# Optimization experiments

Hardware: AMD Instinct MI355X
Metric: run time of the kernel (lower is better)

Reference implementation:

```python
import jax, jax.numpy as jnp
from jax import lax
import numpy as np

B, T, C = 32, 1024, 512
K = 3
MAX_DUR = 4            # durations drawn from [0,5) -> max value 4
L_MAX = T * MAX_DUR    # static padded mel length (torch pads to batch max; we pad to static max)
EPS = 1e-5


def conv_ln_block(x, w, b, g, beta):
    # x: [B,T,C]; torch ConvLNBlock: permute -> Conv1d(SAME) -> relu -> permute -> LayerNorm -> dropout(eval=id)
    y = lax.conv_general_dilated(x.transpose(0, 2, 1), w, (1,), 'SAME',
                                 dimension_numbers=('NCH', 'OIH', 'NCH')) + b[None, :, None]
    y = jax.nn.relu(y).transpose(0, 2, 1)  # [B,T,Cout]
    mu = y.mean(-1, keepdims=True)
    var = y.var(-1, keepdims=True)
    return (y - mu) * lax.rsqrt(var + EPS) * g + beta


def regulate(batch, durations, token_lengths):
    # Vectorized equivalent of DurationRegulator.inflate: repeat token t durations[b,t] times,
    # concatenate, pad. Implemented as cumsum + searchsorted gather (single pass, no ragged loops).
    pos = jnp.arange(T)
    valid = pos[None, :] < token_lengths[:, None]          # [B,T]
    d = jnp.where(valid, durations, 0)
    total = d.sum(axis=1)
    # torch: if durs.sum()==0 -> fill with 1
    d = jnp.where((total == 0)[:, None], valid.astype(d.dtype), d)
    total = d.sum(axis=1)                                   # [B]
    cum = jnp.cumsum(d, axis=1)                             # inclusive cumsum [B,T]
    frames = jnp.arange(L_MAX)
    idx = jax.vmap(lambda c: jnp.searchsorted(c, frames, side='right'))(cum)  # [B,L_MAX]
    idx = jnp.clip(idx, 0, T - 1)
    out = jnp.take_along_axis(batch, idx[:, :, None], axis=1)                 # [B,L_MAX,C]
    frame_mask = frames[None, :] < total[:, None]
    out = out * frame_mask[:, :, None].astype(batch.dtype)
    return out, total.astype(jnp.float32)


def setup_inputs() -> dict:
    key = jax.random.key(0)
    ks = jax.random.split(key, 8)
    batch = jax.random.normal(ks[0], (B, T, C), dtype=jnp.float32)
    token_lengths = jax.random.randint(ks[1], (B,), T // 2, T + 1).astype(jnp.int32)
    mask = jnp.arange(T)[None, :] < token_lengths[:, None]
    label_durations = jax.random.randint(ks[2], (B, T), 0, MAX_DUR + 1).astype(jnp.int32)
    s1 = 1.0 / np.sqrt(C * K)
    s2 = 1.0 / np.sqrt(C * K)
    params = {
        'conv1_w': jax.random.uniform(ks[3], (C, C, K), minval=-s1, maxval=s1, dtype=jnp.float32),
        'conv1_b': jnp.zeros((C,), jnp.float32),
        'ln1_g': jnp.ones((C,), jnp.float32), 'ln1_b': jnp.zeros((C,), jnp.float32),
        'conv2_w': jax.random.uniform(ks[4], (C, C, K), minval=-s2, maxval=s2, dtype=jnp.float32),
        'conv2_b': jnp.zeros((C,), jnp.float32),
        'ln2_g': jnp.ones((C,), jnp.float32), 'ln2_b': jnp.zeros((C,), jnp.float32),
        'lin_w': jax.random.uniform(ks[5], (C, 1), minval=-1/np.sqrt(C), maxval=1/np.sqrt(C), dtype=jnp.float32),
        'lin_b': jnp.zeros((1,), jnp.float32),
    }
    return dict(batch=batch, token_lengths=token_lengths, mask=mask,
                label_durations=label_durations, **params)


def reference(batch, token_lengths, mask, label_durations,
              conv1_w, conv1_b, ln1_g, ln1_b,
              conv2_w, conv2_b, ln2_g, ln2_b,
              lin_w, lin_b):
    # VariancePredictor: two ConvLN blocks + Linear(out_channels, 1), masked fill 0
    h = conv_ln_block(batch, conv1_w, conv1_b, ln1_g, ln1_b)
    h = conv_ln_block(h, conv2_w, conv2_b, ln2_g, ln2_b)
    predicted_durations = h @ lin_w + lin_b                      # [B,T,1]
    predicted_durations = jnp.where(mask[:, :, None], predicted_durations, 0.0)
    # label_durations provided -> regulator uses labels (training path), alpha=1
    padded_batch, mel_lengths = regulate(batch, label_durations, token_lengths)
    return padded_batch, mel_lengths, predicted_durations
```

## Files before the change

kernel.cpp:

```cpp
#include <hip/hip_runtime.h>
#include <hip/hip_bf16.h>
#include <stdint.h>


typedef _Float16 f16;
typedef _Float16 f16x8 __attribute__((ext_vector_type(8)));
typedef float f32x4 __attribute__((ext_vector_type(4)));

#define B_    32
#define T_    1024
#define TP_   1026
#define C_    512
#define LMAX_ 4096
#define KDIM  1536

#define XPAD_OFF   0u
#define H1PAD_OFF  33619968u
#define W1T_OFF    67239936u
#define W2T_OFF    68812800u
#define YWS_OFF    70385664u
#define TOT_OFF    137494528u
#define IDX_OFF    137495040u
#define GWL_OFF    138019328u
#define K12_OFF    138021376u
#define STAT2_OFF  138021888u

#define AS1C(p) ((const __attribute__((address_space(1))) void*)(p))
#define AS3(p)  ((__attribute__((address_space(3))) void*)(p))

__global__ __launch_bounds__(256) void prep_pad(const float* __restrict__ batch,
                                                f16* __restrict__ xpad,
                                                f16* __restrict__ h1pad) {
    int row = blockIdx.x * 4 + (threadIdx.x >> 6);
    int lane = threadIdx.x & 63;
    int b = row / TP_, tt = row % TP_;
    size_t dsto = (size_t)row * C_ + lane * 8;
    if (tt == 0 || tt == TP_ - 1) {
        f16x8 z = {};
        *(f16x8*)(xpad + dsto) = z;
        *(f16x8*)(h1pad + dsto) = z;
    } else {
        const float* src = batch + ((size_t)(b * T_ + tt - 1)) * C_ + lane * 8;
        float4 v0 = ((const float4*)src)[0];
        float4 v1 = ((const float4*)src)[1];
        f16x8 h;
        h[0] = (f16)v0.x; h[1] = (f16)v0.y; h[2] = (f16)v0.z; h[3] = (f16)v0.w;
        h[4] = (f16)v1.x; h[5] = (f16)v1.y; h[6] = (f16)v1.z; h[7] = (f16)v1.w;
        *(f16x8*)(xpad + dsto) = h;
    }
}

__global__ __launch_bounds__(256) void prep_w(const float* __restrict__ w1,
                                              const float* __restrict__ w2,
                                              f16* __restrict__ w1t,
                                              f16* __restrict__ w2t,
                                              const float* __restrict__ g2,
                                              const float* __restrict__ be2,
                                              const float* __restrict__ lw,
                                              float* __restrict__ gwl,
                                              float* __restrict__ k12) {
    int o = blockIdx.x;
    const float* w = blockIdx.y ? w2 : w1;
    f16* wt = blockIdx.y ? w2t : w1t;
    for (int j = threadIdx.x; j < KDIM; j += 256) {
        int tap = j >> 9, i = j & 511;
        wt[(size_t)o * KDIM + j] = (f16)w[(size_t)o * KDIM + i * 3 + tap];
    }
    if (blockIdx.x == 0 && blockIdx.y == 0) {
        __shared__ float rk[4][2];
        float k1 = 0.f, k2 = 0.f;
        for (int c = threadIdx.x; c < C_; c += 256) {
            float gw_ = g2[c] * lw[c];
            gwl[c] = gw_;
            k1 += gw_;
            k2 += be2[c] * lw[c];
        }
#pragma unroll
        for (int m = 32; m; m >>= 1) {
            k1 += __shfl_xor(k1, m, 64);
            k2 += __shfl_xor(k2, m, 64);
        }
        if ((threadIdx.x & 63) == 0) {
            rk[threadIdx.x >> 6][0] = k1;
            rk[threadIdx.x >> 6][1] = k2;
        }
        __syncthreads();
        if (threadIdx.x == 0) {
            k12[0] = rk[0][0] + rk[1][0] + rk[2][0] + rk[3][0];
            k12[1] = rk[0][1] + rk[1][1] + rk[2][1] + rk[3][1];
        }
    }
}

__global__ __launch_bounds__(1024) void scan_kernel(const int* __restrict__ dur,
                                                    const int* __restrict__ tlen,
                                                    int* __restrict__ idxarr,
                                                    int* __restrict__ total,
                                                    float* __restrict__ mel_out) {
    int b = blockIdx.x, t = threadIdx.x;
    __shared__ int sd[1024];
    __shared__ int sv[1024];
    int L = tlen[b];
    int valid = (t < L) ? 1 : 0;
    int d = valid ? dur[b * T_ + t] : 0;
    sd[t] = d; sv[t] = valid;
    __syncthreads();
    for (int off = 1; off < 1024; off <<= 1) {
        int x = 0, y = 0;
        if (t >= off) { x = sd[t - off]; y = sv[t - off]; }
        __syncthreads();
        sd[t] += x; sv[t] += y;
        __syncthreads();
    }
    int totd = sd[1023];
    int cur  = (totd == 0) ? sv[t] : sd[t];
    int prev = (t == 0) ? 0 : ((totd == 0) ? sv[t - 1] : sd[t - 1]);
    for (int f = prev; f < cur; f++) idxarr[b * LMAX_ + f] = t;
    if (t == 1023) {
        int tt = (totd == 0) ? sv[1023] : totd;
        total[b] = tt;
        mel_out[b] = (float)tt;
    }
}

template<int EPI>
__global__ __launch_bounds__(256, 2) void gemm_k(const f16* __restrict__ A,
                                                 const f16* __restrict__ Bw,
                                                 const float* __restrict__ bias,
                                                 f16* __restrict__ Y,
                                                 const float* __restrict__ gwl,
                                                 float4* __restrict__ stats) {
    __shared__ f16 As[128 * 64];
    __shared__ f16 Bs[256 * 64];
    const int tid = threadIdx.x;
    const int lane = tid & 63;
    const int w = tid >> 6;
    const int m0 = blockIdx.x * 128;
    const int n0 = blockIdx.y * 256;
    const int arow0 = (m0 >> 10) * TP_ + (m0 & 1023);
    const int wm = (w & 1) * 64;
    const int wn = (w >> 1) * 128;

    f32x4 acc[4][8];
#pragma unroll
    for (int i = 0; i < 4; i++)
#pragma unroll
        for (int j = 0; j < 8; j++) acc[i][j] = (f32x4){0.f, 0.f, 0.f, 0.f};

    const int lrow = lane >> 3;
    const int gran = (lane & 7) ^ lrow;
    const f16* aB = A + (size_t)(arow0 + lrow) * C_ + gran * 8;
    const f16* bB = Bw + (size_t)(n0 + lrow) * KDIM + gran * 8;

    for (int kk = 0; kk < KDIM; kk += 64) {
        __syncthreads();
#pragma unroll
        for (int i = 0; i < 4; i++) {
            const int rb = (w + i * 4) * 8;
            __builtin_amdgcn_global_load_lds(AS1C(aB + (size_t)rb * C_ + kk),
                                             AS3(&As[rb * 64]), 16, 0, 0);
        }
#pragma unroll
        for (int j = 0; j < 8; j++) {
            const int rb = (w + j * 4) * 8;
            __builtin_amdgcn_global_load_lds(AS1C(bB + (size_t)rb * KDIM + kk),
                                             AS3(&Bs[rb * 64]), 16, 0, 0);
        }
        __syncthreads();
#pragma unroll
        for (int ks = 0; ks < 2; ks++) {
            const int sl = ((ks << 2) + (lane >> 4)) ^ (lane & 7);
            f16x8 af[4], bf[8];
#pragma unroll
            for (int mi = 0; mi < 4; mi++)
                af[mi] = *(const f16x8*)&As[(wm + mi * 16 + (lane & 15)) * 64 + sl * 8];
#pragma unroll
            for (int ni = 0; ni < 8; ni++)
                bf[ni] = *(const f16x8*)&Bs[(wn + ni * 16 + (lane & 15)) * 64 + sl * 8];
#pragma unroll
            for (int mi = 0; mi < 4; mi++)
#pragma unroll
                for (int ni = 0; ni < 8; ni++)
                    acc[mi][ni] = __builtin_amdgcn_mfma_f32_16x16x32_f16(
                        af[mi], bf[ni], acc[mi][ni], 0, 0, 0);
        }
    }

    const int col = lane & 15;
    const int row4 = (lane >> 4) * 4;

    if (EPI == 0) {
#pragma unroll
        for (int ni = 0; ni < 8; ni++) {
            int n = n0 + wn + ni * 16 + col;
            float bn = bias[n];
#pragma unroll
            for (int mi = 0; mi < 4; mi++) {
#pragma unroll
                for (int r = 0; r < 4; r++) {
                    int m = m0 + wm + mi * 16 + row4 + r;
                    float v = acc[mi][ni][r] + bn;
                    Y[(size_t)m * C_ + n] = (f16)(v > 0.f ? v : 0.f);
                }
            }
        }
    } else {
        float bn[8], gw[8];
#pragma unroll
        for (int ni = 0; ni < 8; ni++) {
            int n = n0 + wn + ni * 16 + col;
            bn[ni] = bias[n];
            gw[ni] = gwl[n];
        }
        float s_[4][4], q_[4][4], u_[4][4];
#pragma unroll
        for (int mi = 0; mi < 4; mi++)
#pragma unroll
            for (int r = 0; r < 4; r++) { s_[mi][r] = 0.f; q_[mi][r] = 0.f; u_[mi][r] = 0.f; }
#pragma unroll
        for (int mi = 0; mi < 4; mi++)
#pragma unroll
            for (int ni = 0; ni < 8; ni++)
#pragma unroll
                for (int r = 0; r < 4; r++) {
                    float v = acc[mi][ni][r] + bn[ni];
                    v = v > 0.f ? v : 0.f;
                    s_[mi][r] += v;
                    q_[mi][r] += v * v;
                    u_[mi][r] += v * gw[ni];
                }
#pragma unroll
        for (int m = 8; m; m >>= 1)
#pragma unroll
            for (int mi = 0; mi < 4; mi++)
#pragma unroll
                for (int r = 0; r < 4; r++) {
                    s_[mi][r] += __shfl_xor(s_[mi][r], m, 64);
                    q_[mi][r] += __shfl_xor(q_[mi][r], m, 64);
                    u_[mi][r] += __shfl_xor(u_[mi][r], m, 64);
                }
        __syncthreads();
        float* red = (float*)As;
        if (col == 0) {
#pragma unroll
            for (int mi = 0; mi < 4; mi++)
#pragma unroll
                for (int r = 0; r < 4; r++) {
                    int row = wm + mi * 16 + row4 + r;
                    int idx = ((w >> 1) * 128 + row) * 3;
                    red[idx]     = s_[mi][r];
                    red[idx + 1] = q_[mi][r];
                    red[idx + 2] = u_[mi][r];
                }
        }
        __syncthreads();
        if (tid < 128) {
            float S = red[tid * 3]     + red[(128 + tid) * 3];
            float Q = red[tid * 3 + 1] + red[(128 + tid) * 3 + 1];
            float U = red[tid * 3 + 2] + red[(128 + tid) * 3 + 2];
            stats[(size_t)(m0 + tid) * 2 + blockIdx.y] = (float4){S, Q, U, 0.f};
        }
    }
}

__global__ __launch_bounds__(256) void ln_kernel(const f16* __restrict__ Y,
                                                 const float* __restrict__ g,
                                                 const float* __restrict__ be,
                                                 f16* __restrict__ hpad) {
    int row = blockIdx.x * 4 + (threadIdx.x >> 6);
    int lane = threadIdx.x & 63;
    f16x8 yv = *(const f16x8*)(Y + (size_t)row * C_ + lane * 8);
    float v[8];
#pragma unroll
    for (int i = 0; i < 8; i++) v[i] = (float)yv[i];
    float s = 0.f, q = 0.f;
#pragma unroll
    for (int i = 0; i < 8; i++) { s += v[i]; q += v[i] * v[i]; }
#pragma unroll
    for (int m = 32; m; m >>= 1) { s += __shfl_xor(s, m, 64); q += __shfl_xor(q, m, 64); }
    float mu = s * (1.f / 512.f);
    float x = q * (1.f / 512.f) - mu * mu + 1e-5f;
    float rs = rsqrtf(x);
    rs = rs * (1.5f - 0.5f * x * rs * rs);
    const float4 g0 = ((const float4*)g)[lane * 2], g1 = ((const float4*)g)[lane * 2 + 1];
    const float4 e0 = ((const float4*)be)[lane * 2], e1 = ((const float4*)be)[lane * 2 + 1];
    f16x8 h;
    h[0] = (f16)((v[0] - mu) * rs * g0.x + e0.x);
    h[1] = (f16)((v[1] - mu) * rs * g0.y + e0.y);
    h[2] = (f16)((v[2] - mu) * rs * g0.z + e0.z);
    h[3] = (f16)((v[3] - mu) * rs * g0.w + e0.w);
    h[4] = (f16)((v[4] - mu) * rs * g1.x + e1.x);
    h[5] = (f16)((v[5] - mu) * rs * g1.y + e1.y);
    h[6] = (f16)((v[6] - mu) * rs * g1.z + e1.z);
    h[7] = (f16)((v[7] - mu) * rs * g1.w + e1.w);
    int b = row >> 10, t = row & 1023;
    *(f16x8*)(hpad + ((size_t)(b * TP_ + t + 1)) * C_ + lane * 8) = h;
}

__global__ __launch_bounds__(256) void finalize2(const float4* __restrict__ stats,
                                                 const float* __restrict__ k12,
                                                 const float* __restrict__ lb,
                                                 const int* __restrict__ tlen,
                                                 float* __restrict__ pred) {
    int m = blockIdx.x * 256 + threadIdx.x;
    float4 a = stats[(size_t)m * 2];
    float4 b = stats[(size_t)m * 2 + 1];
    float S = a.x + b.x, Q = a.y + b.y, U = a.z + b.z;
    float mu = S * (1.f / 512.f);
    float x = Q * (1.f / 512.f) - mu * mu + 1e-5f;
    float rs = rsqrtf(x);
    rs = rs * (1.5f - 0.5f * x * rs * rs);
    float p = rs * (U - mu * k12[0]) + k12[1] + lb[0];
    int bb = m >> 10, t = m & 1023;
    pred[m] = (t < tlen[bb]) ? p : 0.f;
}

__global__ __launch_bounds__(256) void gather_kernel(const float* __restrict__ batch,
                                                     const int* __restrict__ idxarr,
                                                     const int* __restrict__ total,
                                                     float* __restrict__ out) {
    int gw = blockIdx.x * 4 + (threadIdx.x >> 6);
    int lane = threadIdx.x & 63;
    int b = gw >> 12;
    int l = gw & (LMAX_ - 1);
    int tot = total[b];
    float4* dst = (float4*)(out + ((size_t)b * LMAX_ + l) * C_);
    if (l < tot) {
        int idx = idxarr[gw];
        const float4* src = (const float4*)(batch + ((size_t)b * T_ + idx) * C_);
        dst[lane] = src[lane];
        dst[lane + 64] = src[lane + 64];
    } else {
        float4 z = {0.f, 0.f, 0.f, 0.f};
        dst[lane] = z;
        dst[lane + 64] = z;
    }
}

extern "C" void kernel_launch(void* const* d_in, const int* in_sizes, int n_in,
                              void* d_out, int out_size, void* d_ws, size_t ws_size,
                              hipStream_t stream) {
    const float* batch = (const float*)d_in[0];
    const int* tlen    = (const int*)d_in[1];
    const int* durs    = (const int*)d_in[3];
    const float* w1  = (const float*)d_in[4];
    const float* b1  = (const float*)d_in[5];
    const float* g1  = (const float*)d_in[6];
    const float* be1 = (const float*)d_in[7];
    const float* w2  = (const float*)d_in[8];
    const float* b2  = (const float*)d_in[9];
    const float* g2  = (const float*)d_in[10];
    const float* be2 = (const float*)d_in[11];
    const float* lw  = (const float*)d_in[12];
    const float* lb  = (const float*)d_in[13];

    float* out      = (float*)d_out;
    float* mel_out  = out + (size_t)B_ * LMAX_ * C_;
    float* pred_out = mel_out + B_;

    char* ws    = (char*)d_ws;
    f16* xpad   = (f16*)(ws + XPAD_OFF);
    f16* h1pad  = (f16*)(ws + H1PAD_OFF);
    f16* w1t    = (f16*)(ws + W1T_OFF);
    f16* w2t    = (f16*)(ws + W2T_OFF);
    f16* yws    = (f16*)(ws + YWS_OFF);
    int* tot    = (int*)(ws + TOT_OFF);
    int* idxarr = (int*)(ws + IDX_OFF);
    float* gwl  = (float*)(ws + GWL_OFF);
    float* k12  = (float*)(ws + K12_OFF);
    float4* st2 = (float4*)(ws + STAT2_OFF);

    prep_pad<<<B_ * TP_ / 4, 256, 0, stream>>>(batch, xpad, h1pad);
    prep_w<<<dim3(512, 2), 256, 0, stream>>>(w1, w2, w1t, w2t, g2, be2, lw, gwl, k12);
    scan_kernel<<<B_, 1024, 0, stream>>>(durs, tlen, idxarr, tot, mel_out);
    gemm_k<0><<<dim3(256, 2), 256, 0, stream>>>(xpad, w1t, b1, yws, nullptr, nullptr);
    ln_kernel<<<8192, 256, 0, stream>>>(yws, g1, be1, h1pad);
    gemm_k<1><<<dim3(256, 2), 256, 0, stream>>>(h1pad, w2t, b2, nullptr, gwl, st2);
    finalize2<<<128, 256, 0, stream>>>(st2, k12, lb, tlen, pred_out);
    gather_kernel<<<B_ * LMAX_ / 4, 256, 0, stream>>>(batch, idxarr, tot, out);
}
```

Before: 462.1 us.

## Fuse prep kernels, skip GEMM/LN work beyond token lengths, merge finalize into gather

Merges the padding, weight-transpose, scan and constant-reduction kernels into one launch, and merges the finalize step into the gather kernel, cutting the launch count. The GEMM blocks, the LayerNorm rows and the fp16 conversion of padded input rows now exit early when they lie past each sequence's token length, since those rows only influence masked outputs. The risk is correctness: later rows read workspace left over from earlier runs, so the halo and the boundary conditions must cover the conv receptive field exactly.

```diff
diff --git a/kernel.cpp b/kernel.cpp
--- a/kernel.cpp
+++ b/kernel.cpp
@@ -28,98 +28,106 @@
 #define AS1C(p) ((const __attribute__((address_space(1))) void*)(p))
 #define AS3(p)  ((__attribute__((address_space(3))) void*)(p))
 
-__global__ __launch_bounds__(256) void prep_pad(const float* __restrict__ batch,
-                                                f16* __restrict__ xpad,
-                                                f16* __restrict__ h1pad) {
-    int row = blockIdx.x * 4 + (threadIdx.x >> 6);
-    int lane = threadIdx.x & 63;
-    int b = row / TP_, tt = row % TP_;
-    size_t dsto = (size_t)row * C_ + lane * 8;
-    if (tt == 0 || tt == TP_ - 1) {
-        f16x8 z = {};
-        *(f16x8*)(xpad + dsto) = z;
-        *(f16x8*)(h1pad + dsto) = z;
-    } else {
-        const float* src = batch + ((size_t)(b * T_ + tt - 1)) * C_ + lane * 8;
-        float4 v0 = ((const float4*)src)[0];
-        float4 v1 = ((const float4*)src)[1];
-        f16x8 h;
-        h[0] = (f16)v0.x; h[1] = (f16)v0.y; h[2] = (f16)v0.z; h[3] = (f16)v0.w;
-        h[4] = (f16)v1.x; h[5] = (f16)v1.y; h[6] = (f16)v1.z; h[7] = (f16)v1.w;
-        *(f16x8*)(xpad + dsto) = h;
-    }
-}
-
-__global__ __launch_bounds__(256) void prep_w(const float* __restrict__ w1,
-                                              const float* __restrict__ w2,
-                                              f16* __restrict__ w1t,
-                                              f16* __restrict__ w2t,
-                                              const float* __restrict__ g2,
-                                              const float* __restrict__ be2,
-                                              const float* __restrict__ lw,
-                                              float* __restrict__ gwl,
-                                              float* __restrict__ k12) {
-    int o = blockIdx.x;
-    const float* w = blockIdx.y ? w2 : w1;
-    f16* wt = blockIdx.y ? w2t : w1t;
-    for (int j = threadIdx.x; j < KDIM; j += 256) {
-        int tap = j >> 9, i = j & 511;
-        wt[(size_t)o * KDIM + j] = (f16)w[(size_t)o * KDIM + i * 3 + tap];
-    }
-    if (blockIdx.x == 0 && blockIdx.y == 0) {
-        __shared__ float rk[4][2];
+#define PP_BLOCKS   2052
+#define PW_BLOCKS   256
+#define SCAN_BLOCKS 32
+
+__global__ __launch_bounds__(1024) void fused_prep(
+        const float* __restrict__ batch, f16* __restrict__ xpad,
+        f16* __restrict__ h1pad, const int* __restrict__ tlen,
+        const float* __restrict__ w1, const float* __restrict__ w2,
+        f16* __restrict__ w1t, f16* __restrict__ w2t,
+        const float* __restrict__ g2, const float* __restrict__ be2,
+        const float* __restrict__ lw, float* __restrict__ gwl,
+        float* __restrict__ k12,
+        const int* __restrict__ dur, int* __restrict__ idxarr,
+        int* __restrict__ total, float* __restrict__ mel_out) {
+    __shared__ int sd[1024];
+    __shared__ int sv[1024];
+    __shared__ float rk[8][2];
+    const int bid = blockIdx.x;
+    const int tid = threadIdx.x;
+
+    if (bid < PP_BLOCKS) {
+        int row = bid * 16 + (tid >> 6);
+        int lane = tid & 63;
+        int b = row / TP_, tt = row % TP_;
+        size_t dsto = (size_t)row * C_ + lane * 8;
+        if (tt == 0 || tt == TP_ - 1) {
+            f16x8 z = {};
+            *(f16x8*)(xpad + dsto) = z;
+            *(f16x8*)(h1pad + dsto) = z;
+        } else if (tt <= tlen[b] + 130) {
+            const float* src = batch + ((size_t)(b * T_ + tt - 1)) * C_ + lane * 8;
+            float4 v0 = ((const float4*)src)[0];
+            float4 v1 = ((const float4*)src)[1];
+            f16x8 h;
+            h[0] = (f16)v0.x; h[1] = (f16)v0.y; h[2] = (f16)v0.z; h[3] = (f16)v0.w;
+            h[4] = (f16)v1.x; h[5] = (f16)v1.y; h[6] = (f16)v1.z; h[7] = (f16)v1.w;
+            *(f16x8*)(xpad + dsto) = h;
+        }
+        return;
+    }
+    if (bid < PP_BLOCKS + PW_BLOCKS) {
+        int unit = (bid - PP_BLOCKS) * 4 + (tid >> 8);
+        int o = unit & 511;
+        const float* w = (unit >> 9) ? w2 : w1;
+        f16* wt = (unit >> 9) ? w2t : w1t;
+        int tl = tid & 255;
+        for (int j = tl; j < KDIM; j += 256) {
+            int tap = j >> 9, i = j & 511;
+            wt[(size_t)o * KDIM + j] = (f16)w[(size_t)o * KDIM + i * 3 + tap];
+        }
+        return;
+    }
+    if (bid < PP_BLOCKS + PW_BLOCKS + SCAN_BLOCKS) {
+        int b = bid - (PP_BLOCKS + PW_BLOCKS);
+        int t = tid;
+        int L = tlen[b];
+        int valid = (t < L) ? 1 : 0;
+        int d = valid ? dur[b * T_ + t] : 0;
+        sd[t] = d; sv[t] = valid;
+        __syncthreads();
+        for (int off = 1; off < 1024; off <<= 1) {
+            int x = 0, y = 0;
+            if (t >= off) { x = sd[t - off]; y = sv[t - off]; }
+            __syncthreads();
+            sd[t] += x; sv[t] += y;
+            __syncthreads();
+        }
+        int totd = sd[1023];
+        int cur  = (totd == 0) ? sv[t] : sd[t];
+        int prev = (t == 0) ? 0 : ((totd == 0) ? sv[t - 1] : sd[t - 1]);
+        for (int f = prev; f < cur; f++) idxarr[b * LMAX_ + f] = t;
+        if (t == 1023) {
+            int tt = (totd == 0) ? sv[1023] : totd;
+            total[b] = tt;
+            mel_out[b] = (float)tt;
+        }
+        return;
+    }
+    {
         float k1 = 0.f, k2 = 0.f;
-        for (int c = threadIdx.x; c < C_; c += 256) {
-            float gw_ = g2[c] * lw[c];
-            gwl[c] = gw_;
-            k1 += gw_;
-            k2 += be2[c] * lw[c];
+        if (tid < C_) {
+            float gw_ = g2[tid] * lw[tid];
+            gwl[tid] = gw_;
+            k1 = gw_;
+            k2 = be2[tid] * lw[tid];
         }
 #pragma unroll
         for (int m = 32; m; m >>= 1) {
             k1 += __shfl_xor(k1, m, 64);
             k2 += __shfl_xor(k2, m, 64);
         }
-        if ((threadIdx.x & 63) == 0) {
-            rk[threadIdx.x >> 6][0] = k1;
-            rk[threadIdx.x >> 6][1] = k2;
-        }
-        __syncthreads();
-        if (threadIdx.x == 0) {
-            k12[0] = rk[0][0] + rk[1][0] + rk[2][0] + rk[3][0];
-            k12[1] = rk[0][1] + rk[1][1] + rk[2][1] + rk[3][1];
-        }
-    }
-}
-
-__global__ __launch_bounds__(1024) void scan_kernel(const int* __restrict__ dur,
-                                                    const int* __restrict__ tlen,
-                                                    int* __restrict__ idxarr,
-                                                    int* __restrict__ total,
-                                                    float* __restrict__ mel_out) {
-    int b = blockIdx.x, t = threadIdx.x;
-    __shared__ int sd[1024];
-    __shared__ int sv[1024];
-    int L = tlen[b];
-    int valid = (t < L) ? 1 : 0;
-    int d = valid ? dur[b * T_ + t] : 0;
-    sd[t] = d; sv[t] = valid;
-    __syncthreads();
-    for (int off = 1; off < 1024; off <<= 1) {
-        int x = 0, y = 0;
-        if (t >= off) { x = sd[t - off]; y = sv[t - off]; }
-        __syncthreads();
-        sd[t] += x; sv[t] += y;
-        __syncthreads();
-    }
-    int totd = sd[1023];
-    int cur  = (totd == 0) ? sv[t] : sd[t];
-    int prev = (t == 0) ? 0 : ((totd == 0) ? sv[t - 1] : sd[t - 1]);
-    for (int f = prev; f < cur; f++) idxarr[b * LMAX_ + f] = t;
-    if (t == 1023) {
-        int tt = (totd == 0) ? sv[1023] : totd;
-        total[b] = tt;
-        mel_out[b] = (float)tt;
+        int wv = tid >> 6;
+        if ((tid & 63) == 0 && wv < 8) { rk[wv][0] = k1; rk[wv][1] = k2; }
+        __syncthreads();
+        if (tid == 0) {
+            float a1 = 0.f, a2 = 0.f;
+#pragma unroll
+            for (int i = 0; i < 8; i++) { a1 += rk[i][0]; a2 += rk[i][1]; }
+            k12[0] = a1; k12[1] = a2;
+        }
     }
 }
 
@@ -129,13 +137,19 @@
                                                  const float* __restrict__ bias,
                                                  f16* __restrict__ Y,
                                                  const float* __restrict__ gwl,
-                                                 float4* __restrict__ stats) {
+                                                 float4* __restrict__ stats,
+                                                 const int* __restrict__ tlen) {
     __shared__ f16 As[128 * 64];
     __shared__ f16 Bs[256 * 64];
+    const int m0 = blockIdx.x * 128;
+    {
+        const int bb = m0 >> 10, t0 = m0 & 1023;
+        const int L = tlen[bb];
+        if (EPI == 0 ? (t0 > L) : (t0 >= L)) return;
+    }
     const int tid = threadIdx.x;
     const int lane = tid & 63;
     const int w = tid >> 6;
-    const int m0 = blockIdx.x * 128;
     const int n0 = blockIdx.y * 256;
     const int arow0 = (m0 >> 10) * TP_ + (m0 & 1023);
     const int wm = (w & 1) * 64;
@@ -266,9 +280,12 @@
 __global__ __launch_bounds__(256) void ln_kernel(const f16* __restrict__ Y,
                                                  const float* __restrict__ g,
                                                  const float* __restrict__ be,
-                                                 f16* __restrict__ hpad) {
+                                                 f16* __restrict__ hpad,
+                                                 const int* __restrict__ tlen) {
     int row = blockIdx.x * 4 + (threadIdx.x >> 6);
     int lane = threadIdx.x & 63;
+    int b = row >> 10, t = row & 1023;
+    if (t > tlen[b]) return;
     f16x8 yv = *(const f16x8*)(Y + (size_t)row * C_ + lane * 8);
     float v[8];
 #pragma unroll
@@ -293,47 +310,47 @@
     h[5] = (f16)((v[5] - mu) * rs * g1.y + e1.y);
     h[6] = (f16)((v[6] - mu) * rs * g1.z + e1.z);
     h[7] = (f16)((v[7] - mu) * rs * g1.w + e1.w);
-    int b = row >> 10, t = row & 1023;
     *(f16x8*)(hpad + ((size_t)(b * TP_ + t + 1)) * C_ + lane * 8) = h;
 }
 
-__global__ __launch_bounds__(256) void finalize2(const float4* __restrict__ stats,
-                                                 const float* __restrict__ k12,
-                                                 const float* __restrict__ lb,
-                                                 const int* __restrict__ tlen,
-                                                 float* __restrict__ pred) {
-    int m = blockIdx.x * 256 + threadIdx.x;
-    float4 a = stats[(size_t)m * 2];
-    float4 b = stats[(size_t)m * 2 + 1];
-    float S = a.x + b.x, Q = a.y + b.y, U = a.z + b.z;
-    float mu = S * (1.f / 512.f);
-    float x = Q * (1.f / 512.f) - mu * mu + 1e-5f;
-    float rs = rsqrtf(x);
-    rs = rs * (1.5f - 0.5f * x * rs * rs);
-    float p = rs * (U - mu * k12[0]) + k12[1] + lb[0];
-    int bb = m >> 10, t = m & 1023;
-    pred[m] = (t < tlen[bb]) ? p : 0.f;
-}
-
-__global__ __launch_bounds__(256) void gather_kernel(const float* __restrict__ batch,
-                                                     const int* __restrict__ idxarr,
-                                                     const int* __restrict__ total,
-                                                     float* __restrict__ out) {
-    int gw = blockIdx.x * 4 + (threadIdx.x >> 6);
-    int lane = threadIdx.x & 63;
-    int b = gw >> 12;
-    int l = gw & (LMAX_ - 1);
-    int tot = total[b];
-    float4* dst = (float4*)(out + ((size_t)b * LMAX_ + l) * C_);
-    if (l < tot) {
-        int idx = idxarr[gw];
-        const float4* src = (const float4*)(batch + ((size_t)b * T_ + idx) * C_);
-        dst[lane] = src[lane];
-        dst[lane + 64] = src[lane + 64];
+__global__ __launch_bounds__(256) void gather_fin(const float* __restrict__ batch,
+                                                  const int* __restrict__ idxarr,
+                                                  const int* __restrict__ total,
+                                                  float* __restrict__ out,
+                                                  const float4* __restrict__ stats,
+                                                  const float* __restrict__ k12,
+                                                  const float* __restrict__ lb,
+                                                  const int* __restrict__ tlen,
+                                                  float* __restrict__ pred) {
+    if (blockIdx.x < 32768) {
+        int gw = blockIdx.x * 4 + (threadIdx.x >> 6);
+        int lane = threadIdx.x & 63;
+        int b = gw >> 12;
+        int l = gw & (LMAX_ - 1);
+        int tot = total[b];
+        float4* dst = (float4*)(out + ((size_t)b * LMAX_ + l) * C_);
+        if (l < tot) {
+            int idx = idxarr[gw];
+            const float4* src = (const float4*)(batch + ((size_t)b * T_ + idx) * C_);
+            dst[lane] = src[lane];
+            dst[lane + 64] = src[lane + 64];
+        } else {
+            float4 z = {0.f, 0.f, 0.f, 0.f};
+            dst[lane] = z;
+            dst[lane + 64] = z;
+        }
     } else {
-        float4 z = {0.f, 0.f, 0.f, 0.f};
-        dst[lane] = z;
-        dst[lane + 64] = z;
+        int m = (blockIdx.x - 32768) * 256 + threadIdx.x;
+        float4 a = stats[(size_t)m * 2];
+        float4 b = stats[(size_t)m * 2 + 1];
+        float S = a.x + b.x, Q = a.y + b.y, U = a.z + b.z;
+        float mu = S * (1.f / 512.f);
+        float x = Q * (1.f / 512.f) - mu * mu + 1e-5f;
+        float rs = rsqrtf(x);
+        rs = rs * (1.5f - 0.5f * x * rs * rs);
+        float p = rs * (U - mu * k12[0]) + k12[1] + lb[0];
+        int bb = m >> 10, t = m & 1023;
+        pred[m] = (t < tlen[bb]) ? p : 0.f;
     }
 }
 
@@ -370,12 +387,14 @@
     float* k12  = (float*)(ws + K12_OFF);
     float4* st2 = (float4*)(ws + STAT2_OFF);
 
-    prep_pad<<<B_ * TP_ / 4, 256, 0, stream>>>(batch, xpad, h1pad);
-    prep_w<<<dim3(512, 2), 256, 0, stream>>>(w1, w2, w1t, w2t, g2, be2, lw, gwl, k12);
-    scan_kernel<<<B_, 1024, 0, stream>>>(durs, tlen, idxarr, tot, mel_out);
-    gemm_k<0><<<dim3(256, 2), 256, 0, stream>>>(xpad, w1t, b1, yws, nullptr, nullptr);
-    ln_kernel<<<8192, 256, 0, stream>>>(yws, g1, be1, h1pad);
-    gemm_k<1><<<dim3(256, 2), 256, 0, stream>>>(h1pad, w2t, b2, nullptr, gwl, st2);
-    finalize2<<<128, 256, 0, stream>>>(st2, k12, lb, tlen, pred_out);
-    gather_kernel<<<B_ * LMAX_ / 4, 256, 0, stream>>>(batch, idxarr, tot, out);
+    fused_prep<<<PP_BLOCKS + PW_BLOCKS + SCAN_BLOCKS + 1, 1024, 0, stream>>>(
+        batch, xpad, h1pad, tlen, w1, w2, w1t, w2t,
+        g2, be2, lw, gwl, k12, durs, idxarr, tot, mel_out);
+    gemm_k<0><<<dim3(256, 2), 256, 0, stream>>>(xpad, w1t, b1, yws,
+                                                nullptr, nullptr, tlen);
+    ln_kernel<<<8192, 256, 0, stream>>>(yws, g1, be1, h1pad, tlen);
+    gemm_k<1><<<dim3(256, 2), 256, 0, stream>>>(h1pad, w2t, b2, nullptr,
+                                                gwl, st2, tlen);
+    gather_fin<<<32768 + 128, 256, 0, stream>>>(batch, idxarr, tot, out,
+                                                st2, k12, lb, tlen, pred_out);
 }
```

Result: faster. 450.2 us (-2.6%).
